# Optimization experiments

Measured on AMD Instinct MI355X. Metric: run time of the kernel, lower is better.

## Reference

```python
import jax, jax.numpy as jnp
import numpy as np


def _conv1x1_relu(x, w, b):
    # x: [B,C,H,W], w: [O,C], b: [O] -> relu(1x1 conv) [B,O,H,W]
    y = jnp.einsum('oc,bchw->bohw', w, x) + b[None, :, None, None]
    return jax.nn.relu(y)


def setup_inputs() -> dict:
    key = jax.random.key(0)
    ks = jax.random.split(key, 9)
    B, C, H, W = 16, 128, 256, 64
    s = 1.0 / np.sqrt(C)
    return {
        'rep': jax.random.normal(ks[0], (B, C, H, W), jnp.float32),
        'wq': jax.random.normal(ks[1], (C, C), jnp.float32) * s,
        'bq': jax.random.normal(ks[2], (C,), jnp.float32) * 0.02,
        'wk': jax.random.normal(ks[3], (C, C), jnp.float32) * s,
        'bk': jax.random.normal(ks[4], (C,), jnp.float32) * 0.02,
        'wv': jax.random.normal(ks[5], (C, C), jnp.float32) * s,
        'bv': jax.random.normal(ks[6], (C,), jnp.float32) * 0.02,
        'wfc': jax.random.normal(ks[7], (C, C), jnp.float32) * s,
        'bfc': jax.random.normal(ks[8], (C,), jnp.float32) * 0.02,
    }


def reference(rep, wq, bq, wk, bk, wv, bv, wfc, bfc):
    C = rep.shape[1]
    # ReLU-activated 1x1-conv Q/K/V projections, then permute to [B,W,H,C]
    q = _conv1x1_relu(rep, wq, bq).transpose(0, 3, 2, 1)  # [B,W,H,C]
    k = _conv1x1_relu(rep, wk, bk).transpose(0, 3, 2, 1)
    v = _conv1x1_relu(rep, wv, bv).transpose(0, 3, 2, 1)
    # attention over the H axis, independently per (B, W)
    attn = jnp.einsum('bwhc,bwgc->bwhg', q, k) / jnp.sqrt(jnp.asarray(C, q.dtype))
    attn = jax.nn.softmax(attn, axis=-1)  # [B,W,H,H]
    out = jnp.einsum('bwhg,bwgc->bwhc', attn, v)  # [B,W,H,C]
    # back to NCHW, final ReLU 1x1 conv
    out = out.transpose(0, 3, 2, 1)  # [B,C,H,W]
    return _conv1x1_relu(out, wfc, bfc)
```

## Files before the change

kernel.cpp:

```cpp
#include <hip/hip_runtime.h>


typedef __attribute__((ext_vector_type(8))) short short8;
typedef __attribute__((ext_vector_type(4))) float f32x4;
typedef __attribute__((ext_vector_type(4))) int int4v;

#define MFMA16(acc, a, b) (acc) = __builtin_amdgcn_mfma_f32_16x16x32_bf16((a), (b), (acc), 0, 0, 0)

__device__ __forceinline__ unsigned short f2b(float f) {
  unsigned u = __builtin_bit_cast(unsigned, f);
  u = (u + 0x7fffu + ((u >> 16) & 1u)) >> 16;
  return (unsigned short)u;
}

__device__ __forceinline__ unsigned adr_s(int r, int c) {
  return (unsigned)(((r << 8) + (c << 1)) ^ ((r & 7) << 4));
}
__device__ __forceinline__ unsigned adr_q(int r, int c) {
  return (unsigned)(((r << 8) + (c << 1)) ^ (((r ^ (r >> 3)) & 7) << 4));
}
__device__ __forceinline__ unsigned adr_vt(int c, int g) {
  unsigned blk = (unsigned)(((g >> 3) ^ (c & 7) ^ ((c >> 3) & 7)) & 31);
  return (unsigned)((c << 9) + (blk << 4) + ((g & 7) << 1));
}
__device__ __forceinline__ unsigned ps_adr(int r, int c) {
  return (unsigned)(((r << 7) + (c << 1)) ^ (((r ^ (r >> 3)) & 7) << 4));
}

__device__ __forceinline__ short8 ldsf(const char* p, unsigned off) {
  return *(const short8*)(p + off);
}

__global__ __launch_bounds__(256) void k0_wcvt(
    const float* __restrict__ wq, const float* __restrict__ wk,
    const float* __restrict__ wv, const float* __restrict__ wfc,
    unsigned short* __restrict__ wb)
{
  int i = blockIdx.x * 256 + threadIdx.x;
  int mat = i >> 12, off = (i & 4095) * 4;
  const float* src = (mat == 0) ? wq : (mat == 1) ? wk : (mat == 2) ? wv : wfc;
  float4 v = *(const float4*)(src + off);
  uint2 u;
  u.x = (unsigned)f2b(v.x) | ((unsigned)f2b(v.y) << 16);
  u.y = (unsigned)f2b(v.z) | ((unsigned)f2b(v.w) << 16);
  *(uint2*)(wb + mat * 16384 + off) = u;
}


__device__ __forceinline__ void k1_one(const unsigned short* wmat, const float* bias,
    unsigned short* dst, const char* XS, char* WS,
    int brel, int n0, int wvid, int l, int l16, int g4) {
  const int strip = wvid * 16;
  short8 wf[4];
#pragma unroll
  for (int kk = 0; kk < 4; ++kk)
    wf[kk] = *(const short8*)(wmat + (strip + l16) * 128 + kk * 32 + g4 * 8);
  float bv4[4];
#pragma unroll
  for (int r = 0; r < 4; ++r) bv4[r] = bias[strip + g4 * 4 + r];

  f32x4 acc[8];
#pragma unroll
  for (int nt = 0; nt < 8; ++nt) acc[nt] = (f32x4){0.f, 0.f, 0.f, 0.f};
#pragma unroll
  for (int nt = 0; nt < 8; ++nt) {
#pragma unroll
    for (int kk = 0; kk < 4; ++kk) {
      short8 xb = ldsf(XS, adr_q(nt * 16 + l16, kk * 32 + g4 * 8));
      MFMA16(acc[nt], wf[kk], xb);
    }
  }
#pragma unroll
  for (int hf = 0; hf < 2; ++hf) {
    __syncthreads();
#pragma unroll
    for (int nt4 = 0; nt4 < 4; ++nt4) {
      int nt = hf * 4 + nt4;
      float y0 = fmaxf(acc[nt][0] + bv4[0], 0.f);
      float y1 = fmaxf(acc[nt][1] + bv4[1], 0.f);
      float y2 = fmaxf(acc[nt][2] + bv4[2], 0.f);
      float y3 = fmaxf(acc[nt][3] + bv4[3], 0.f);
      uint2 u;
      u.x = (unsigned)f2b(y0) | ((unsigned)f2b(y1) << 16);
      u.y = (unsigned)f2b(y2) | ((unsigned)f2b(y3) << 16);
      int row = nt4 * 16 + l16;
      unsigned cb = (unsigned)(wvid * 32 + g4 * 8);
      *(uint2*)(WS + (unsigned)(row << 8) + (cb ^ ((unsigned)(row & 7) << 4))) = u;
    }
    __syncthreads();
#pragma unroll
    for (int it = 0; it < 8; ++it) {
      int row = it * 8 + wvid;
      unsigned u = *(const unsigned*)(WS + (unsigned)(row << 8) +
                                     (((unsigned)(l << 2)) ^ ((unsigned)(row & 7) << 4)));
      int n = n0 + hf * 64 + row;
      int h = n >> 6, w = n & 63;
      ((unsigned*)dst)[(size_t)((brel * 64 + w) * 256 + h) * 64 + l] = u;
    }
  }
}

__global__ __launch_bounds__(512, 4) void k1_qkv(
    const float* __restrict__ rep, const unsigned short* __restrict__ wb,
    const float* __restrict__ bq, const float* __restrict__ bk,
    const float* __restrict__ bv,
    unsigned short* __restrict__ qo, unsigned short* __restrict__ ko,
    unsigned short* __restrict__ vo, int b0)
{
  extern __shared__ char smem[];
  char* XS = smem;
  char* WS = smem + (32 << 10);

  const int t = threadIdx.x;
  const int wvid = t >> 6, l = t & 63, l16 = l & 15, g4 = l >> 4;
  const int brel = blockIdx.x >> 7;
  const int n0 = (blockIdx.x & 127) * 128;
  const int b = b0 + brel;

#pragma unroll
  for (int it = 0; it < 8; ++it) {
    int i = it * 512 + t;
    int c = i >> 5, j4 = i & 31;
    float4 xv = *(const float4*)(rep + (size_t)(b * 128 + c) * 16384 + n0 + j4 * 4);
    float vv[4] = {xv.x, xv.y, xv.z, xv.w};
#pragma unroll
    for (int r = 0; r < 4; ++r)
      *(unsigned short*)(XS + adr_q(j4 * 4 + r, c)) = f2b(vv[r]);
  }
  __syncthreads();

  k1_one(wb,         bq, qo, XS, WS, brel, n0, wvid, l, l16, g4);
  k1_one(wb + 16384, bk, ko, XS, WS, brel, n0, wvid, l, l16, g4);
  k1_one(wb + 32768, bv, vo, XS, WS, brel, n0, wvid, l, l16, g4);
}


__global__ __launch_bounds__(1024, 1) void k2_attn(
    const unsigned short* __restrict__ qws, const unsigned short* __restrict__ kws,
    const unsigned short* __restrict__ vws, unsigned short* __restrict__ aws)
{
  extern __shared__ char smem[];
  char* KS  = smem;
  char* VTS = smem + (64 << 10);

  const int t = threadIdx.x;
  const int wvid = t >> 6, l = t & 63, l16 = l & 15, g4 = l >> 4;
  char* PS = smem + (128 << 10) + (wvid << 11);

  const int brel = blockIdx.x >> 6;
  const int w = blockIdx.x & 63;
  const size_t wbase = (size_t)((brel * 64 + w)) * 256;

  const int hb = wvid * 16;

  short8 qa[4];
#pragma unroll
  for (int kk = 0; kk < 4; ++kk)
    qa[kk] = *(const short8*)(qws + (wbase + hb + l16) * 128 + kk * 32 + g4 * 8);

#pragma unroll
  for (int it = 0; it < 4; ++it) {
    int i = it * 1024 + t;
    int g = i >> 4, c16 = i & 15;
    int gp = (g & ~31) | ((g & 4) << 2) | ((g >> 1) & 12) | (g & 3);
    short8 kv = *(const short8*)(kws + (wbase + g) * 128 + c16 * 8);
    *(short8*)(KS + adr_s(gp, c16 * 8)) = kv;
  }
#pragma unroll
  for (int it = 0; it < 4; ++it) {
    int i = it * 1024 + t;
    int g = i >> 4, c16 = i & 15;
    short8 vv = *(const short8*)(vws + (wbase + g) * 128 + c16 * 8);
#pragma unroll
    for (int j = 0; j < 8; ++j)
      *(unsigned short*)(VTS + adr_vt(c16 * 8 + j, g)) = (unsigned short)vv[j];
  }
  __syncthreads();

  const float SCL2 = 0.08838834764831845f * 1.4426950408889634f;

  f32x4 sc[16];
#pragma unroll
  for (int gt = 0; gt < 16; ++gt) {
    f32x4 acc = {0.f, 0.f, 0.f, 0.f};
#pragma unroll
    for (int kk = 0; kk < 4; ++kk) {
      short8 kb = ldsf(KS, adr_s(gt * 16 + l16, kk * 32 + g4 * 8));
      MFMA16(acc, kb, qa[kk]);
    }
    sc[gt] = acc;
  }

  float mm = fmaxf(fmaxf(sc[0][0], sc[0][1]), fmaxf(sc[0][2], sc[0][3]));
#pragma unroll
  for (int gt = 1; gt < 16; ++gt) {
    float m4 = fmaxf(fmaxf(sc[gt][0], sc[gt][1]), fmaxf(sc[gt][2], sc[gt][3]));
    mm = fmaxf(mm, m4);
  }
  mm = fmaxf(mm, __shfl_xor(mm, 16, 64));
  mm = fmaxf(mm, __shfl_xor(mm, 32, 64));
  const float mneg = -mm * SCL2;
  float s = 0.f;
#pragma unroll
  for (int gt = 0; gt < 16; ++gt) {
#pragma unroll
    for (int r = 0; r < 4; ++r) {
      float p = exp2f(fmaf(sc[gt][r], SCL2, mneg));
      sc[gt][r] = p;
      s += p;
    }
  }
  s += __shfl_xor(s, 16, 64);
  s += __shfl_xor(s, 32, 64);
  const float rcp = 1.0f / s;

  unsigned pk0[16], pk1[16];
#pragma unroll
  for (int gt = 0; gt < 16; ++gt) {
    pk0[gt] = (unsigned)f2b(sc[gt][0] * rcp) | ((unsigned)f2b(sc[gt][1] * rcp) << 16);
    pk1[gt] = (unsigned)f2b(sc[gt][2] * rcp) | ((unsigned)f2b(sc[gt][3] * rcp) << 16);
  }

  f32x4 oacc[8];
#pragma unroll
  for (int nt = 0; nt < 8; ++nt) oacc[nt] = (f32x4){0.f, 0.f, 0.f, 0.f};
#pragma unroll
  for (int kks = 0; kks < 8; ++kks) {
    int4v pv = {(int)pk0[2 * kks], (int)pk1[2 * kks],
                (int)pk0[2 * kks + 1], (int)pk1[2 * kks + 1]};
    short8 pa = __builtin_bit_cast(short8, pv);
#pragma unroll
    for (int nt = 0; nt < 8; ++nt) {
      short8 vb = ldsf(VTS, adr_vt(nt * 16 + l16, kks * 32 + g4 * 8));
      MFMA16(oacc[nt], pa, vb);
    }
  }

#pragma unroll
  for (int ch = 0; ch < 2; ++ch) {
#pragma unroll
    for (int nt4 = 0; nt4 < 4; ++nt4) {
      int nt = ch * 4 + nt4;
#pragma unroll
      for (int r = 0; r < 4; ++r)
        *(unsigned short*)(PS + ps_adr(g4 * 4 + r, nt4 * 16 + l16)) = f2b(oacc[nt][r]);
    }
#pragma unroll
    for (int it = 0; it < 8; ++it) {
      int row = it * 2 + (l >> 5);
      int cd  = l & 31;
      unsigned base = (unsigned)(row << 7) +
          (((unsigned)(cd << 2)) ^ (((unsigned)((row ^ (row >> 3)) & 7)) << 4));
      unsigned lo = *(const unsigned short*)(PS + base);
      unsigned hi = *(const unsigned short*)(PS + base + 2);
      ((unsigned*)aws)[(wbase + hb + row) * 64 + ch * 32 + cd] = lo | (hi << 16);
    }
  }
}


__global__ __launch_bounds__(512, 4) void k3_conv(
    const unsigned short* __restrict__ aws, const unsigned short* __restrict__ wb,
    const float* __restrict__ bfc, float* __restrict__ out, int b0)
{
  extern __shared__ char smem[];
  char* AS = smem;

  const int t = threadIdx.x;
  const int wvid = t >> 6, l = t & 63, l16 = l & 15, g4 = l >> 4;
  (void)l;
  const int brel = blockIdx.x >> 6;
  const int n0 = (blockIdx.x & 63) * 256;
  const int b = b0 + brel;

#pragma unroll
  for (int it = 0; it < 8; ++it) {
    int i = it * 512 + t;
    int nn = i >> 4, c16 = i & 15;
    int n = n0 + nn;
    int h = n >> 6, w = n & 63;
    short8 av = *(const short8*)(aws + ((size_t)((brel * 64 + w) * 256 + h)) * 128 + c16 * 8);
    *(short8*)(AS + adr_s(nn, c16 * 8)) = av;
  }
  __syncthreads();

  const int strip = wvid * 16;
  const unsigned short* wfcb = wb + 3 * 16384;
  short8 wf[4];
#pragma unroll
  for (int kk = 0; kk < 4; ++kk)
    wf[kk] = *(const short8*)(wfcb + (strip + l16) * 128 + kk * 32 + g4 * 8);
  float bv4[4];
#pragma unroll
  for (int r = 0; r < 4; ++r) bv4[r] = bfc[strip + g4 * 4 + r];

#pragma unroll
  for (int nt = 0; nt < 16; ++nt) {
    f32x4 acc = {0.f, 0.f, 0.f, 0.f};
#pragma unroll
    for (int kk = 0; kk < 4; ++kk) {
      short8 ab = ldsf(AS, adr_s(nt * 16 + l16, kk * 32 + g4 * 8));
      MFMA16(acc, wf[kk], ab);
    }
#pragma unroll
    for (int r = 0; r < 4; ++r) {
      int o = strip + g4 * 4 + r;
      out[(size_t)(b * 128 + o) * 16384 + n0 + nt * 16 + l16] = fmaxf(acc[r] + bv4[r], 0.f);
    }
  }
}

extern "C" void kernel_launch(void* const* d_in, const int* in_sizes, int n_in,
                              void* d_out, int out_size, void* d_ws, size_t ws_size,
                              hipStream_t stream) {
  const float* rep = (const float*)d_in[0];
  const float* wq  = (const float*)d_in[1];
  const float* bq  = (const float*)d_in[2];
  const float* wk  = (const float*)d_in[3];
  const float* bk  = (const float*)d_in[4];
  const float* wv  = (const float*)d_in[5];
  const float* bv  = (const float*)d_in[6];
  const float* wfc = (const float*)d_in[7];
  const float* bfc = (const float*)d_in[8];
  float* out = (float*)d_out;
  (void)in_sizes; (void)n_in; (void)out_size;

  hipFuncSetAttribute((const void*)k1_qkv,  hipFuncAttributeMaxDynamicSharedMemorySize, 48 * 1024);
  hipFuncSetAttribute((const void*)k2_attn, hipFuncAttributeMaxDynamicSharedMemorySize, 160 * 1024);
  hipFuncSetAttribute((const void*)k3_conv, hipFuncAttributeMaxDynamicSharedMemorySize, 64 * 1024);

  const size_t wb_bytes = 4 * 16384 * 2;
  const size_t per_b = (size_t)16384 * 128 * 2;
  if (ws_size < wb_bytes + 4 * per_b) return;
  size_t nb_max = (ws_size - wb_bytes) / (4 * per_b);
  int nb = (int)(nb_max < 16 ? nb_max : 16);

  char* ws = (char*)d_ws;
  unsigned short* qws = (unsigned short*)(ws);
  unsigned short* kws = (unsigned short*)(ws + (size_t)nb * per_b);
  unsigned short* vws = (unsigned short*)(ws + (size_t)nb * per_b * 2);
  unsigned short* aws = (unsigned short*)(ws + (size_t)nb * per_b * 3);
  unsigned short* wb  = (unsigned short*)(ws + (size_t)nb * per_b * 4);

  k0_wcvt<<<dim3(64), dim3(256), 0, stream>>>(wq, wk, wv, wfc, wb);

  for (int b0 = 0; b0 < 16; b0 += nb) {
    int nbc = (16 - b0) < nb ? (16 - b0) : nb;
    k1_qkv<<<dim3(nbc * 128), dim3(512), 48 * 1024, stream>>>(
        rep, wb, bq, bk, bv, qws, kws, vws, b0);
    k2_attn<<<dim3(nbc * 64), dim3(1024), 160 * 1024, stream>>>(qws, kws, vws, aws);
    k3_conv<<<dim3(nbc * 64), dim3(512), 64 * 1024, stream>>>(aws, wb, bfc, out, b0);
  }
}
```

Before: 234.4 us.

## Process two query row tiles per wave in attention kernel with 512 threads

```diff
diff --git a/kernel.cpp b/kernel.cpp
--- a/kernel.cpp
+++ b/kernel.cpp
@@ -135,7 +135,7 @@
 }
 
 
-__global__ __launch_bounds__(1024, 1) void k2_attn(
+__global__ __launch_bounds__(512, 2) void k2_attn(
     const unsigned short* __restrict__ qws, const unsigned short* __restrict__ kws,
     const unsigned short* __restrict__ vws, unsigned short* __restrict__ aws)
 {
@@ -151,24 +151,27 @@
   const int w = blockIdx.x & 63;
   const size_t wbase = (size_t)((brel * 64 + w)) * 256;
 
-  const int hb = wvid * 16;
-
-  short8 qa[4];
-#pragma unroll
-  for (int kk = 0; kk < 4; ++kk)
-    qa[kk] = *(const short8*)(qws + (wbase + hb + l16) * 128 + kk * 32 + g4 * 8);
-
-#pragma unroll
-  for (int it = 0; it < 4; ++it) {
-    int i = it * 1024 + t;
+  const int hb0 = wvid * 32;
+  const int hb1 = wvid * 32 + 16;
+
+  short8 qa0[4], qa1[4];
+#pragma unroll
+  for (int kk = 0; kk < 4; ++kk) {
+    qa0[kk] = *(const short8*)(qws + (wbase + hb0 + l16) * 128 + kk * 32 + g4 * 8);
+    qa1[kk] = *(const short8*)(qws + (wbase + hb1 + l16) * 128 + kk * 32 + g4 * 8);
+  }
+
+#pragma unroll
+  for (int it = 0; it < 8; ++it) {
+    int i = it * 512 + t;
     int g = i >> 4, c16 = i & 15;
     int gp = (g & ~31) | ((g & 4) << 2) | ((g >> 1) & 12) | (g & 3);
     short8 kv = *(const short8*)(kws + (wbase + g) * 128 + c16 * 8);
     *(short8*)(KS + adr_s(gp, c16 * 8)) = kv;
   }
 #pragma unroll
-  for (int it = 0; it < 4; ++it) {
-    int i = it * 1024 + t;
+  for (int it = 0; it < 8; ++it) {
+    int i = it * 512 + t;
     int g = i >> 4, c16 = i & 15;
     short8 vv = *(const short8*)(vws + (wbase + g) * 128 + c16 * 8);
 #pragma unroll
@@ -179,81 +182,127 @@
 
   const float SCL2 = 0.08838834764831845f * 1.4426950408889634f;
 
-  f32x4 sc[16];
+  f32x4 sc0[16], sc1[16];
 #pragma unroll
   for (int gt = 0; gt < 16; ++gt) {
-    f32x4 acc = {0.f, 0.f, 0.f, 0.f};
+    f32x4 a0 = {0.f, 0.f, 0.f, 0.f};
+    f32x4 a1 = {0.f, 0.f, 0.f, 0.f};
 #pragma unroll
     for (int kk = 0; kk < 4; ++kk) {
       short8 kb = ldsf(KS, adr_s(gt * 16 + l16, kk * 32 + g4 * 8));
-      MFMA16(acc, kb, qa[kk]);
-    }
-    sc[gt] = acc;
-  }
-
-  float mm = fmaxf(fmaxf(sc[0][0], sc[0][1]), fmaxf(sc[0][2], sc[0][3]));
-#pragma unroll
-  for (int gt = 1; gt < 16; ++gt) {
-    float m4 = fmaxf(fmaxf(sc[gt][0], sc[gt][1]), fmaxf(sc[gt][2], sc[gt][3]));
-    mm = fmaxf(mm, m4);
-  }
-  mm = fmaxf(mm, __shfl_xor(mm, 16, 64));
-  mm = fmaxf(mm, __shfl_xor(mm, 32, 64));
-  const float mneg = -mm * SCL2;
-  float s = 0.f;
-#pragma unroll
-  for (int gt = 0; gt < 16; ++gt) {
-#pragma unroll
-    for (int r = 0; r < 4; ++r) {
-      float p = exp2f(fmaf(sc[gt][r], SCL2, mneg));
-      sc[gt][r] = p;
-      s += p;
-    }
-  }
-  s += __shfl_xor(s, 16, 64);
-  s += __shfl_xor(s, 32, 64);
-  const float rcp = 1.0f / s;
-
-  unsigned pk0[16], pk1[16];
-#pragma unroll
-  for (int gt = 0; gt < 16; ++gt) {
-    pk0[gt] = (unsigned)f2b(sc[gt][0] * rcp) | ((unsigned)f2b(sc[gt][1] * rcp) << 16);
-    pk1[gt] = (unsigned)f2b(sc[gt][2] * rcp) | ((unsigned)f2b(sc[gt][3] * rcp) << 16);
-  }
-
-  f32x4 oacc[8];
-#pragma unroll
-  for (int nt = 0; nt < 8; ++nt) oacc[nt] = (f32x4){0.f, 0.f, 0.f, 0.f};
+      MFMA16(a0, kb, qa0[kk]);
+      MFMA16(a1, kb, qa1[kk]);
+    }
+    sc0[gt] = a0;
+    sc1[gt] = a1;
+  }
+
+  unsigned pk0a[16], pk1a[16];
+  {
+    float mm = fmaxf(fmaxf(sc0[0][0], sc0[0][1]), fmaxf(sc0[0][2], sc0[0][3]));
+#pragma unroll
+    for (int gt = 1; gt < 16; ++gt) {
+      float m4 = fmaxf(fmaxf(sc0[gt][0], sc0[gt][1]), fmaxf(sc0[gt][2], sc0[gt][3]));
+      mm = fmaxf(mm, m4);
+    }
+    mm = fmaxf(mm, __shfl_xor(mm, 16, 64));
+    mm = fmaxf(mm, __shfl_xor(mm, 32, 64));
+    const float mneg = -mm * SCL2;
+    float s = 0.f;
+#pragma unroll
+    for (int gt = 0; gt < 16; ++gt) {
+#pragma unroll
+      for (int r = 0; r < 4; ++r) {
+        float p = exp2f(fmaf(sc0[gt][r], SCL2, mneg));
+        sc0[gt][r] = p;
+        s += p;
+      }
+    }
+    s += __shfl_xor(s, 16, 64);
+    s += __shfl_xor(s, 32, 64);
+    const float rcp = 1.0f / s;
+#pragma unroll
+    for (int gt = 0; gt < 16; ++gt) {
+      pk0a[gt] = (unsigned)f2b(sc0[gt][0] * rcp) | ((unsigned)f2b(sc0[gt][1] * rcp) << 16);
+      pk1a[gt] = (unsigned)f2b(sc0[gt][2] * rcp) | ((unsigned)f2b(sc0[gt][3] * rcp) << 16);
+    }
+  }
+  unsigned pk0b[16], pk1b[16];
+  {
+    float mm = fmaxf(fmaxf(sc1[0][0], sc1[0][1]), fmaxf(sc1[0][2], sc1[0][3]));
+#pragma unroll
+    for (int gt = 1; gt < 16; ++gt) {
+      float m4 = fmaxf(fmaxf(sc1[gt][0], sc1[gt][1]), fmaxf(sc1[gt][2], sc1[gt][3]));
+      mm = fmaxf(mm, m4);
+    }
+    mm = fmaxf(mm, __shfl_xor(mm, 16, 64));
+    mm = fmaxf(mm, __shfl_xor(mm, 32, 64));
+    const float mneg = -mm * SCL2;
+    float s = 0.f;
+#pragma unroll
+    for (int gt = 0; gt < 16; ++gt) {
+#pragma unroll
+      for (int r = 0; r < 4; ++r) {
+        float p = exp2f(fmaf(sc1[gt][r], SCL2, mneg));
+        sc1[gt][r] = p;
+        s += p;
+      }
+    }
+    s += __shfl_xor(s, 16, 64);
+    s += __shfl_xor(s, 32, 64);
+    const float rcp = 1.0f / s;
+#pragma unroll
+    for (int gt = 0; gt < 16; ++gt) {
+      pk0b[gt] = (unsigned)f2b(sc1[gt][0] * rcp) | ((unsigned)f2b(sc1[gt][1] * rcp) << 16);
+      pk1b[gt] = (unsigned)f2b(sc1[gt][2] * rcp) | ((unsigned)f2b(sc1[gt][3] * rcp) << 16);
+    }
+  }
+
+  f32x4 oacc0[8], oacc1[8];
+#pragma unroll
+  for (int nt = 0; nt < 8; ++nt) {
+    oacc0[nt] = (f32x4){0.f, 0.f, 0.f, 0.f};
+    oacc1[nt] = (f32x4){0.f, 0.f, 0.f, 0.f};
+  }
 #pragma unroll
   for (int kks = 0; kks < 8; ++kks) {
-    int4v pv = {(int)pk0[2 * kks], (int)pk1[2 * kks],
-                (int)pk0[2 * kks + 1], (int)pk1[2 * kks + 1]};
-    short8 pa = __builtin_bit_cast(short8, pv);
+    int4v pv0 = {(int)pk0a[2 * kks], (int)pk1a[2 * kks],
+                 (int)pk0a[2 * kks + 1], (int)pk1a[2 * kks + 1]};
+    int4v pv1 = {(int)pk0b[2 * kks], (int)pk1b[2 * kks],
+                 (int)pk0b[2 * kks + 1], (int)pk1b[2 * kks + 1]};
+    short8 pa0 = __builtin_bit_cast(short8, pv0);
+    short8 pa1 = __builtin_bit_cast(short8, pv1);
 #pragma unroll
     for (int nt = 0; nt < 8; ++nt) {
       short8 vb = ldsf(VTS, adr_vt(nt * 16 + l16, kks * 32 + g4 * 8));
-      MFMA16(oacc[nt], pa, vb);
-    }
-  }
-
-#pragma unroll
-  for (int ch = 0; ch < 2; ++ch) {
-#pragma unroll
-    for (int nt4 = 0; nt4 < 4; ++nt4) {
-      int nt = ch * 4 + nt4;
-#pragma unroll
-      for (int r = 0; r < 4; ++r)
-        *(unsigned short*)(PS + ps_adr(g4 * 4 + r, nt4 * 16 + l16)) = f2b(oacc[nt][r]);
-    }
-#pragma unroll
-    for (int it = 0; it < 8; ++it) {
-      int row = it * 2 + (l >> 5);
-      int cd  = l & 31;
-      unsigned base = (unsigned)(row << 7) +
-          (((unsigned)(cd << 2)) ^ (((unsigned)((row ^ (row >> 3)) & 7)) << 4));
-      unsigned lo = *(const unsigned short*)(PS + base);
-      unsigned hi = *(const unsigned short*)(PS + base + 2);
-      ((unsigned*)aws)[(wbase + hb + row) * 64 + ch * 32 + cd] = lo | (hi << 16);
+      MFMA16(oacc0[nt], pa0, vb);
+      MFMA16(oacc1[nt], pa1, vb);
+    }
+  }
+
+#pragma unroll
+  for (int m = 0; m < 2; ++m) {
+    const int hb = (m == 0) ? hb0 : hb1;
+#pragma unroll
+    for (int ch = 0; ch < 2; ++ch) {
+#pragma unroll
+      for (int nt4 = 0; nt4 < 4; ++nt4) {
+        int nt = ch * 4 + nt4;
+        f32x4 ov = (m == 0) ? oacc0[nt] : oacc1[nt];
+#pragma unroll
+        for (int r = 0; r < 4; ++r)
+          *(unsigned short*)(PS + ps_adr(g4 * 4 + r, nt4 * 16 + l16)) = f2b(ov[r]);
+      }
+#pragma unroll
+      for (int it = 0; it < 8; ++it) {
+        int row = it * 2 + (l >> 5);
+        int cd  = l & 31;
+        unsigned base = (unsigned)(row << 7) +
+            (((unsigned)(cd << 2)) ^ (((unsigned)((row ^ (row >> 3)) & 7)) << 4));
+        unsigned lo = *(const unsigned short*)(PS + base);
+        unsigned hi = *(const unsigned short*)(PS + base + 2);
+        ((unsigned*)aws)[(wbase + hb + row) * 64 + ch * 32 + cd] = lo | (hi << 16);
+      }
     }
   }
 }
@@ -326,7 +375,7 @@
   (void)in_sizes; (void)n_in; (void)out_size;
 
   hipFuncSetAttribute((const void*)k1_qkv,  hipFuncAttributeMaxDynamicSharedMemorySize, 48 * 1024);
-  hipFuncSetAttribute((const void*)k2_attn, hipFuncAttributeMaxDynamicSharedMemorySize, 160 * 1024);
+  hipFuncSetAttribute((const void*)k2_attn, hipFuncAttributeMaxDynamicSharedMemorySize, 144 * 1024);
   hipFuncSetAttribute((const void*)k3_conv, hipFuncAttributeMaxDynamicSharedMemorySize, 64 * 1024);
 
   const size_t wb_bytes = 4 * 16384 * 2;
@@ -348,7 +397,7 @@
     int nbc = (16 - b0) < nb ? (16 - b0) : nb;
     k1_qkv<<<dim3(nbc * 128), dim3(512), 48 * 1024, stream>>>(
         rep, wb, bq, bk, bv, qws, kws, vws, b0);
-    k2_attn<<<dim3(nbc * 64), dim3(1024), 160 * 1024, stream>>>(qws, kws, vws, aws);
+    k2_attn<<<dim3(nbc * 64), dim3(512), 144 * 1024, stream>>>(qws, kws, vws, aws);
     k3_conv<<<dim3(nbc * 64), dim3(512), 64 * 1024, stream>>>(aws, wb, bfc, out, b0);
   }
 }
```

Result: faster. 229.0 us (-2.3%).
